# Performance work log

Measured on AMD Instinct MI355X. Metric: run time of the kernel, lower is better.

Reference implementation:

```python
import jax, jax.numpy as jnp
import numpy as np

BLANK = 0
NEG = -1e30  # effective -inf that avoids nan from inf - inf


def setup_inputs() -> dict:
    key = jax.random.key(0)
    k1, k2, k3, k4 = jax.random.split(key, 4)
    B, T, U, V = 8, 256, 64, 1024
    logits = jax.random.normal(k1, (B, T, U + 1, V), dtype=jnp.float32)
    targets = jax.random.randint(k2, (B, U), 1, V)          # labels (avoid blank)
    input_lengths = jax.random.randint(k3, (B,), T // 2, T + 1)
    target_lengths = jax.random.randint(k4, (B,), U // 2, U + 1)
    return {
        "logits": logits,
        "targets": targets,
        "input_lengths": input_lengths,
        "target_lengths": target_lengths,
    }


def _rnnt_loss(logits, targets, input_lengths, target_lengths):
    # logits: (B, T, U+1, V). Standard RNN-T forward (alpha) recursion:
    #   alpha[t, u] = logaddexp(alpha[t-1, u] + blank[t-1, u],
    #                           alpha[t, u-1] + y[t, u-1])
    # loss_b = -(alpha[T_b-1, U_b] + blank[T_b-1, U_b])
    B, T, U1, V = logits.shape
    U = U1 - 1
    lp = jax.nn.log_softmax(logits, axis=-1)
    blank_lp = lp[..., BLANK]                                   # (B, T, U+1)
    # emission log-prob of target label at each (t, u), u in [0, U)
    y = jnp.take_along_axis(lp[:, :, :U, :], targets[:, None, :, None], axis=-1)[..., 0]
    u_em = jnp.arange(U)
    y = jnp.where(u_em[None, None, :] < target_lengths[:, None, None], y, NEG)
    # exclusive cumsum along u: c[b, t, u] = sum_{k<u} y[b, t, k]   (B, T, U+1)
    c = jnp.concatenate([jnp.zeros((B, T, 1), lp.dtype), jnp.cumsum(y, axis=-1)], axis=-1)
    valid_u = jnp.arange(U1)[None, :] <= target_lengths[:, None]  # (B, U+1)
    # t = 0 row: alpha[0, u] = sum_{k<u} y[0, k]
    alpha0 = jnp.where(valid_u, c[:, 0, :], NEG)
    # Within a time step, alpha[t, u] = c[u] + logcumsumexp_u(a[u'] - c[u'])
    # where a[u'] = alpha[t-1, u'] + blank[t-1, u'] -> parallel over u.
    blank_seq = jnp.moveaxis(blank_lp[:, :-1, :], 1, 0)          # (T-1, B, U+1)
    c_seq = jnp.moveaxis(c[:, 1:, :], 1, 0)                      # (T-1, B, U+1)

    def step(alpha, xs):
        b_prev, c_t = xs
        a = alpha + b_prev
        z = jax.lax.associative_scan(jnp.logaddexp, a - c_t, axis=1)
        alpha_new = jnp.where(valid_u, c_t + z, NEG)
        return alpha_new, alpha_new

    _, alphas = jax.lax.scan(step, alpha0, (blank_seq, c_seq))
    all_alpha = jnp.concatenate([alpha0[None], alphas], axis=0)  # (T, B, U+1)
    bidx = jnp.arange(B)
    a_fin = all_alpha[input_lengths - 1, bidx, target_lengths]
    b_fin = blank_lp[bidx, input_lengths - 1, target_lengths]
    ll = a_fin + b_fin
    return jnp.mean(-ll)  # reduction='mean' over batch (torchaudio semantics)


def reference(logits, targets, input_lengths, target_lengths):
    return _rnnt_loss(logits, targets, input_lengths, target_lengths)
```

## Files before the change

kernel.cpp:

```cpp
#include <hip/hip_runtime.h>
#include <math.h>

#define NEG -1e30f
#define LOG2E 1.4426950408889634f
#define LN2 0.6931471805599453f

__device__ __forceinline__ float shup1(float x, float lane0val) {
    return __int_as_float(__builtin_amdgcn_update_dpp(
        __float_as_int(lane0val), __float_as_int(x), 0x138, 0xF, 0xF, false));
}

__device__ __forceinline__ float lae2(float x, float y) {
    float m = fmaxf(x, y);
    float dm = fminf(x, y) - m;
    return m + __builtin_amdgcn_logf(1.f + __builtin_amdgcn_exp2f(dm));
}

__global__ __launch_bounds__(256) void lse_kernel(
    const float* __restrict__ logits,
    const int* __restrict__ targets,
    float* __restrict__ blank_d,
    float* __restrict__ y_d,
    int B, int T, int U, int V) {
    const int wave = threadIdx.x >> 6;
    const int lane = threadIdx.x & 63;
    const long long row = (long long)blockIdx.x * 4 + wave;
    const long long nrows = (long long)B * T * (U + 1);
    if (row >= nrows) return;
    const float* base = logits + row * (long long)V;

    float4 d4[4];
#pragma unroll
    for (int c = 0; c < 4; ++c)
        d4[c] = reinterpret_cast<const float4*>(base)[c * 64 + lane];
    float s = 0.f;
#pragma unroll
    for (int c = 0; c < 4; ++c) {
        s += __builtin_amdgcn_exp2f(d4[c].x * LOG2E) +
             __builtin_amdgcn_exp2f(d4[c].y * LOG2E) +
             __builtin_amdgcn_exp2f(d4[c].z * LOG2E) +
             __builtin_amdgcn_exp2f(d4[c].w * LOG2E);
    }
#pragma unroll
    for (int off = 32; off; off >>= 1) s += __shfl_xor(s, off, 64);

    if (lane == 0) {
        const float l2s = __builtin_amdgcn_logf(s);
        const int U1 = U + 1;
        const int D = T + U;
        const int u = (int)(row % U1);
        const long long bt = row / U1;
        const int b = (int)(bt / T);
        const int t = (int)(bt % T);
        blank_d[((long long)b * D + (t + u)) * U1 + u] = d4[0].x * LOG2E - l2s;
        if (u < U) {
            const int tgt = targets[b * U + u];
            y_d[((long long)b * D + (t + u)) * U + u] = base[tgt] * LOG2E - l2s;
        }
    }
}

__global__ __launch_bounds__(64) void alpha_diag_kernel(
    const float* __restrict__ blank_d,
    const float* __restrict__ y_d,
    const int* __restrict__ in_len,
    const int* __restrict__ tgt_len,
    float* __restrict__ partials,
    int B, int T, int U) {
    const int b = blockIdx.x;
    const int lane = threadIdx.x & 63;
    const int D = T + U;
    const int P1 = U + 1;
    const int Dm1 = D - 1;

    const int Tb = in_len[b];
    const int L = tgt_len[b];
    const float* bd = blank_d + (long long)b * D * P1;
    const float* yd = y_d + (long long)b * D * U;
    const int dstar = Tb - 1 + L;

    float val = NEG;
    float v0 = 0.f;
    const bool yok = (lane < L);

    const int R = 16;
    float bv[R], yv[R], b0[R];
#pragma unroll
    for (int s = 0; s < R; ++s) {
        int r = s; if (r > Dm1) r = Dm1;
        bv[s] = bd[r * P1 + lane + 1];
        yv[s] = yok ? yd[r * U + lane] : NEG;
        b0[s] = bd[r * P1];
    }

    int d = 1;
    for (; d + R - 1 <= dstar; d += R) {
#pragma unroll
        for (int s = 0; s < R; ++s) {
            const float pv = val;
            const float ps = shup1(pv, v0);
            val = lae2(pv + bv[s], ps + yv[s]);
            v0 += b0[s];
            int r = d + s + R - 1;
            if (r > Dm1) r = Dm1;
            bv[s] = bd[r * P1 + lane + 1];
            yv[s] = yok ? yd[r * U + lane] : NEG;
            b0[s] = bd[r * P1];
        }
    }
#pragma unroll
    for (int s = 0; s < R; ++s) {
        if (d + s <= dstar) {
            const float pv = val;
            const float ps = shup1(pv, v0);
            val = lae2(pv + bv[s], ps + yv[s]);
            v0 += b0[s];
        }
    }

    const float aL = __shfl(val, L - 1, 64);
    const float bfin = bd[(long long)dstar * P1 + L];
    if (lane == 0) partials[b] = aL + bfin;
}

__global__ void finish_kernel(const float* __restrict__ partials,
                              float* __restrict__ out, int B) {
    if (threadIdx.x == 0) {
        float s = 0.f;
        for (int w = 0; w < B; ++w) s += partials[w];
        out[0] = -LN2 * s / (float)B;
    }
}

extern "C" void kernel_launch(void* const* d_in, const int* in_sizes, int n_in,
                              void* d_out, int out_size, void* d_ws, size_t ws_size,
                              hipStream_t stream) {
    const float* logits  = (const float*)d_in[0];
    const int* targets   = (const int*)d_in[1];
    const int* in_len    = (const int*)d_in[2];
    const int* tgt_len   = (const int*)d_in[3];

    const int B = in_sizes[2];
    const int U = in_sizes[1] / B;
    const int V = 1024;
    const int T = (int)((long long)in_sizes[0] / ((long long)B * (U + 1) * V));
    const int D = T + U;

    float* partials = (float*)d_ws;
    float* blank_d = partials + 64;
    float* y_d = blank_d + (long long)B * D * (U + 1);

    const long long rows = (long long)B * T * (U + 1);
    const int blocks = (int)((rows + 3) / 4);

    hipLaunchKernelGGL(lse_kernel, dim3(blocks), dim3(256), 0, stream,
                       logits, targets, blank_d, y_d, B, T, U, V);
    hipLaunchKernelGGL(alpha_diag_kernel, dim3(B), dim3(64), 0, stream,
                       blank_d, y_d, in_len, tgt_len, partials, B, T, U);
    hipLaunchKernelGGL(finish_kernel, dim3(1), dim3(64), 0, stream,
                       partials, (float*)d_out, B);
}
```

Measured before the change: 116.3 us.

## Fuse log-softmax and alpha recursion with per-diagonal readiness counters

```diff
diff --git a/kernel.cpp b/kernel.cpp
--- a/kernel.cpp
+++ b/kernel.cpp
@@ -4,6 +4,8 @@
 #define NEG -1e30f
 #define LOG2E 1.4426950408889634f
 #define LN2 0.6931471805599453f
+
+typedef long long ll;
 
 __device__ __forceinline__ float shup1(float x, float lane0val) {
     return __int_as_float(__builtin_amdgcn_update_dpp(
@@ -16,120 +18,151 @@
     return m + __builtin_amdgcn_logf(1.f + __builtin_amdgcn_exp2f(dm));
 }
 
-__global__ __launch_bounds__(256) void lse_kernel(
-    const float* __restrict__ logits,
-    const int* __restrict__ targets,
-    float* __restrict__ blank_d,
-    float* __restrict__ y_d,
-    int B, int T, int U, int V) {
-    const int wave = threadIdx.x >> 6;
+__device__ __forceinline__ void st_coh(float* p, float v) {
+    __hip_atomic_store(p, v, __ATOMIC_RELAXED, __HIP_MEMORY_SCOPE_AGENT);
+}
+__device__ __forceinline__ float ld_coh(const float* p) {
+    return __hip_atomic_load(p, __ATOMIC_RELAXED, __HIP_MEMORY_SCOPE_AGENT);
+}
+__device__ __forceinline__ int ld_cnt(const int* p) {
+    return __hip_atomic_load(p, __ATOMIC_RELAXED, __HIP_MEMORY_SCOPE_AGENT);
+}
+
+__device__ __forceinline__ int ndiag(int r, int T, int U) {
+    int lo = r - U; if (lo < 0) lo = 0;
+    int hi = (r < T - 1) ? r : (T - 1);
+    return hi - lo + 1;
+}
+
+__device__ __forceinline__ void wait_rows(const int* dcnt_b, int lo, int n,
+                                          int Dm1, int T, int U) {
     const int lane = threadIdx.x & 63;
-    const long long row = (long long)blockIdx.x * 4 + wave;
-    const long long nrows = (long long)B * T * (U + 1);
-    if (row >= nrows) return;
-    const float* base = logits + row * (long long)V;
-
-    float4 d4[4];
-#pragma unroll
-    for (int c = 0; c < 4; ++c)
-        d4[c] = reinterpret_cast<const float4*>(base)[c * 64 + lane];
-    float s = 0.f;
-#pragma unroll
-    for (int c = 0; c < 4; ++c) {
-        s += __builtin_amdgcn_exp2f(d4[c].x * LOG2E) +
-             __builtin_amdgcn_exp2f(d4[c].y * LOG2E) +
-             __builtin_amdgcn_exp2f(d4[c].z * LOG2E) +
-             __builtin_amdgcn_exp2f(d4[c].w * LOG2E);
-    }
-#pragma unroll
-    for (int off = 32; off; off >>= 1) s += __shfl_xor(s, off, 64);
-
-    if (lane == 0) {
-        const float l2s = __builtin_amdgcn_logf(s);
-        const int U1 = U + 1;
-        const int D = T + U;
-        const int u = (int)(row % U1);
-        const long long bt = row / U1;
-        const int b = (int)(bt / T);
-        const int t = (int)(bt % T);
-        blank_d[((long long)b * D + (t + u)) * U1 + u] = d4[0].x * LOG2E - l2s;
-        if (u < U) {
-            const int tgt = targets[b * U + u];
-            y_d[((long long)b * D + (t + u)) * U + u] = base[tgt] * LOG2E - l2s;
-        }
+    const bool need = lane < n;
+    int rr = lo + lane; if (rr > Dm1) rr = Dm1;
+    const int want = ndiag(rr, T, U);
+    for (int it = 0; it < 16384; ++it) {
+        bool ok = true;
+        if (need) ok = (ld_cnt(&dcnt_b[rr]) >= want);
+        if (__all(ok)) break;
+        __builtin_amdgcn_s_sleep(2);
     }
 }
 
-__global__ __launch_bounds__(64) void alpha_diag_kernel(
-    const float* __restrict__ blank_d,
-    const float* __restrict__ y_d,
+__global__ __launch_bounds__(256) void fused_kernel(
+    const float* __restrict__ logits,
+    const int* __restrict__ targets,
     const int* __restrict__ in_len,
     const int* __restrict__ tgt_len,
-    float* __restrict__ partials,
-    int B, int T, int U) {
-    const int b = blockIdx.x;
-    const int lane = threadIdx.x & 63;
+    float* blank_d, float* y_d, int* dcnt, float* out,
+    int B, int T, int U, int V) {
+    const int U1 = U + 1;
     const int D = T + U;
-    const int P1 = U + 1;
     const int Dm1 = D - 1;
 
+    if (blockIdx.x >= (unsigned)B) {
+        const int wave = threadIdx.x >> 6;
+        const int lane = threadIdx.x & 63;
+        const ll row = (ll)(blockIdx.x - B) * 4 + wave;
+        const ll nrows = (ll)B * T * U1;
+        if (row >= nrows) return;
+        const float* base = logits + row * (ll)V;
+
+        float4 d4[4];
+#pragma unroll
+        for (int c = 0; c < 4; ++c)
+            d4[c] = reinterpret_cast<const float4*>(base)[c * 64 + lane];
+        float s = 0.f;
+#pragma unroll
+        for (int c = 0; c < 4; ++c) {
+            s += __builtin_amdgcn_exp2f(d4[c].x * LOG2E) +
+                 __builtin_amdgcn_exp2f(d4[c].y * LOG2E) +
+                 __builtin_amdgcn_exp2f(d4[c].z * LOG2E) +
+                 __builtin_amdgcn_exp2f(d4[c].w * LOG2E);
+        }
+#pragma unroll
+        for (int off = 32; off; off >>= 1) s += __shfl_xor(s, off, 64);
+
+        if (lane == 0) {
+            const float l2s = __builtin_amdgcn_logf(s);
+            const int u = (int)(row % U1);
+            const ll bt = row / U1;
+            const int b = (int)(bt / T);
+            const int t = (int)(bt % T);
+            const int dd = t + u;
+            st_coh(&blank_d[((ll)b * D + dd) * U1 + u], d4[0].x * LOG2E - l2s);
+            if (u < U) {
+                const int tgt = targets[b * U + u];
+                st_coh(&y_d[((ll)b * D + dd) * U + u], base[tgt] * LOG2E - l2s);
+            }
+            asm volatile("s_waitcnt vmcnt(0)" ::: "memory");
+            __hip_atomic_fetch_add(&dcnt[b * D + dd], 1,
+                                   __ATOMIC_RELAXED, __HIP_MEMORY_SCOPE_AGENT);
+        }
+        return;
+    }
+
+    if (threadIdx.x >= 64) return;
+    const int b = blockIdx.x;
+    const int lane = threadIdx.x;
     const int Tb = in_len[b];
     const int L = tgt_len[b];
-    const float* bd = blank_d + (long long)b * D * P1;
-    const float* yd = y_d + (long long)b * D * U;
+    const float* bd = blank_d + (ll)b * D * U1;
+    const float* yd = y_d + (ll)b * D * U;
+    const int* db = dcnt + b * D;
     const int dstar = Tb - 1 + L;
 
     float val = NEG;
     float v0 = 0.f;
+    const int u = lane + 1;
     const bool yok = (lane < L);
 
     const int R = 16;
     float bv[R], yv[R], b0[R];
+    wait_rows(db, 0, R, Dm1, T, U);
 #pragma unroll
     for (int s = 0; s < R; ++s) {
-        int r = s; if (r > Dm1) r = Dm1;
-        bv[s] = bd[r * P1 + lane + 1];
-        yv[s] = yok ? yd[r * U + lane] : NEG;
-        b0[s] = bd[r * P1];
+        int r = (s > Dm1) ? Dm1 : s;
+        bv[s] = ld_coh(&bd[r * U1 + u]);
+        yv[s] = yok ? ld_coh(&yd[r * U + lane]) : NEG;
+        b0[s] = ld_coh(&bd[r * U1]);
     }
 
     int d = 1;
     for (; d + R - 1 <= dstar; d += R) {
+        wait_rows(db, d + R - 1, R, Dm1, T, U);
 #pragma unroll
         for (int s = 0; s < R; ++s) {
+            const int dd = d + s;
             const float pv = val;
             const float ps = shup1(pv, v0);
-            val = lae2(pv + bv[s], ps + yv[s]);
+            const float t2 = ps + yv[s];
+            const float nv = lae2(pv + bv[s], t2);
+            val = (dd == u) ? t2 : nv;
             v0 += b0[s];
-            int r = d + s + R - 1;
+            int r = dd + R - 1;
             if (r > Dm1) r = Dm1;
-            bv[s] = bd[r * P1 + lane + 1];
-            yv[s] = yok ? yd[r * U + lane] : NEG;
-            b0[s] = bd[r * P1];
+            bv[s] = ld_coh(&bd[r * U1 + u]);
+            yv[s] = yok ? ld_coh(&yd[r * U + lane]) : NEG;
+            b0[s] = ld_coh(&bd[r * U1]);
         }
     }
 #pragma unroll
     for (int s = 0; s < R; ++s) {
         if (d + s <= dstar) {
+            const int dd = d + s;
             const float pv = val;
             const float ps = shup1(pv, v0);
-            val = lae2(pv + bv[s], ps + yv[s]);
+            const float t2 = ps + yv[s];
+            const float nv = lae2(pv + bv[s], t2);
+            val = (dd == u) ? t2 : nv;
             v0 += b0[s];
         }
     }
 
     const float aL = __shfl(val, L - 1, 64);
-    const float bfin = bd[(long long)dstar * P1 + L];
-    if (lane == 0) partials[b] = aL + bfin;
-}
-
-__global__ void finish_kernel(const float* __restrict__ partials,
-                              float* __restrict__ out, int B) {
-    if (threadIdx.x == 0) {
-        float s = 0.f;
-        for (int w = 0; w < B; ++w) s += partials[w];
-        out[0] = -LN2 * s / (float)B;
-    }
+    const float bfin = ld_coh(&bd[(ll)dstar * U1 + L]);
+    if (lane == 0)
+        atomicAdd(out, -LN2 * (aL + bfin) / (float)B);
 }
 
 extern "C" void kernel_launch(void* const* d_in, const int* in_sizes, int n_in,
@@ -143,20 +176,19 @@
     const int B = in_sizes[2];
     const int U = in_sizes[1] / B;
     const int V = 1024;
-    const int T = (int)((long long)in_sizes[0] / ((long long)B * (U + 1) * V));
+    const int T = (int)((ll)in_sizes[0] / ((ll)B * (U + 1) * V));
     const int D = T + U;
 
-    float* partials = (float*)d_ws;
-    float* blank_d = partials + 64;
-    float* y_d = blank_d + (long long)B * D * (U + 1);
+    int* dcnt = (int*)d_ws;
+    float* blank_d = (float*)(dcnt + (ll)B * D);
+    float* y_d = blank_d + (ll)B * D * (U + 1);
 
-    const long long rows = (long long)B * T * (U + 1);
-    const int blocks = (int)((rows + 3) / 4);
+    const ll rows = (ll)B * T * (U + 1);
+    const int lse_blocks = (int)((rows + 3) / 4);
 
-    hipLaunchKernelGGL(lse_kernel, dim3(blocks), dim3(256), 0, stream,
-                       logits, targets, blank_d, y_d, B, T, U, V);
-    hipLaunchKernelGGL(alpha_diag_kernel, dim3(B), dim3(64), 0, stream,
-                       blank_d, y_d, in_len, tgt_len, partials, B, T, U);
-    hipLaunchKernelGGL(finish_kernel, dim3(1), dim3(64), 0, stream,
-                       partials, (float*)d_out, B);
+    hipMemsetAsync(dcnt, 0, (size_t)B * D * sizeof(int), stream);
+    hipMemsetAsync(d_out, 0, sizeof(float), stream);
+    hipLaunchKernelGGL(fused_kernel, dim3(B + lse_blocks), dim3(256), 0, stream,
+                       logits, targets, in_len, tgt_len,
+                       blank_d, y_d, dcnt, (float*)d_out, B, T, U, V);
 }
```

Result: slower. 178.2 us (+53.2%).
